# Kernel optimization log

Hardware: AMD Instinct MI355X
Metric: run time of the kernel (lower is better)

The kernel has to match this reference:

```python
import jax, jax.numpy as jnp
import numpy as np

HEADS = 6
PS = 7  # window size
DN = ('NCHW', 'OIHW', 'NCHW')


def _conv1x1(x, w):
    return jax.lax.conv_general_dilated(x, w, (1, 1), 'VALID', dimension_numbers=DN)


def _dwconv3(x, w, groups):
    return jax.lax.conv_general_dilated(x, w, (1, 1), 'SAME', dimension_numbers=DN,
                                        feature_group_count=groups)


def _l2norm(t, eps=1e-12):
    # matches torch F.normalize(dim=-1): x / max(||x||_2, eps)
    n = jnp.sqrt(jnp.sum(t * t, axis=-1, keepdims=True))
    return t / jnp.maximum(n, eps)


def setup_inputs() -> dict:
    key = jax.random.key(0)
    k1, k2, k3, k4 = jax.random.split(key, 4)
    B, C, H, W = 2, 180, 448, 448
    x = jax.random.normal(k1, (B, C, H, W), dtype=jnp.float32)
    temperature = jnp.ones((HEADS, 1, 1), dtype=jnp.float32)
    w_qkv = jax.random.normal(k2, (3 * C, C, 1, 1), dtype=jnp.float32) * 0.05
    w_dw = jax.random.normal(k3, (3 * C, 1, 3, 3), dtype=jnp.float32) * 0.05
    w_proj = jax.random.normal(k4, (C, C, 1, 1), dtype=jnp.float32) * 0.05
    return {'x': x, 'temperature': temperature, 'w_qkv': w_qkv, 'w_dw': w_dw, 'w_proj': w_proj}


def reference(x, temperature, w_qkv, w_dw, w_proj):
    b, c, H, W = x.shape
    d = c // HEADS
    hh, ww = H // PS, W // PS

    qkv = _dwconv3(_conv1x1(x, w_qkv), w_dw, 3 * c)  # [b, 3c, H, W]
    q, k, v = jnp.split(qkv, 3, axis=1)

    def rearr(t):
        # 'b (head d) (h ph) (w pw) -> b (h w) head d (ph pw)'
        t = t.reshape(b, HEADS, d, hh, PS, ww, PS)
        t = t.transpose(0, 3, 5, 1, 2, 4, 6)  # b, hh, ww, head, d, ph, pw
        return t.reshape(b, hh * ww, HEADS, d, PS * PS)

    q, k, v = rearr(q), rearr(k), rearr(v)
    q = _l2norm(q)
    k = _l2norm(k)

    # channel-channel attention per window: [b, n_win, head, d, d]
    attn = jnp.einsum('bnhdp,bnhep->bnhde', q, k) * temperature
    attn = jax.nn.softmax(attn, axis=-1)
    out = jnp.einsum('bnhde,bnhep->bnhdp', attn, v)

    # inverse rearrange: 'b (h w) head d (ph pw) -> b (head d) (h ph) (w pw)'
    out = out.reshape(b, hh, ww, HEADS, d, PS, PS)
    out = out.transpose(0, 3, 4, 1, 5, 2, 6).reshape(b, c, H, W)
    return _conv1x1(out, w_proj)
```

## Files before the change

kernel.cpp:

```cpp
#include <hip/hip_runtime.h>

#define HW 200704
#define WIMG 448
#define VPLANE 229376

typedef __attribute__((ext_vector_type(4))) unsigned int u32x4;
typedef __attribute__((ext_vector_type(4))) float f32x4;
typedef __attribute__((ext_vector_type(8))) short s16x8;

static __device__ __forceinline__ unsigned short f2bf(float f) {
    union { float f; unsigned int u; } v; v.f = f;
    unsigned int u = v.u;
    unsigned int r = u + 0x7FFFu + ((u >> 16) & 1u);
    return (unsigned short)(r >> 16);
}
static __device__ __forceinline__ float bf2f(unsigned short s) {
    union { unsigned int u; float f; } v; v.u = ((unsigned int)s) << 16;
    return v.f;
}

__global__ __launch_bounds__(256) void wconv_kernel(
    const float* __restrict__ wq, unsigned short* __restrict__ wqb)
{
    int idx = blockIdx.x * 256 + threadIdx.x;
    if (idx >= 576 * 24) return;
    int row = idx / 24, ch = idx - row * 24;
    unsigned short u[8];
#pragma unroll
    for (int e = 0; e < 8; ++e) {
        int k = ch * 8 + e;
        u[e] = (row < 540 && k < 180) ? f2bf(wq[row * 180 + k]) : (unsigned short)0;
    }
    *(u32x4*)(wqb + row * 192 + ch * 8) = *(const u32x4*)u;
}

__global__ __launch_bounds__(256) void transpose_cast_kernel(
    const float* __restrict__ x, unsigned short* __restrict__ xT)
{
    const int p0 = blockIdx.x * 64;
    const int tid = threadIdx.x;
    const int pl = tid & 63;

    __shared__ float T[180 * 65];

    for (int ic = tid >> 6; ic < 180; ic += 4)
        T[ic * 65 + pl] = x[(size_t)ic * HW + p0 + pl];
    __syncthreads();

    const int cg = tid >> 6;
    unsigned short* drow = xT + ((size_t)p0 + pl) * 192;
#pragma unroll
    for (int i = 0; i < 6; ++i) {
        int k0 = (cg * 6 + i) * 8;
        unsigned short u[8];
#pragma unroll
        for (int e = 0; e < 8; ++e)
            u[e] = (k0 + e < 180) ? f2bf(T[(k0 + e) * 65 + pl]) : (unsigned short)0;
        *(u32x4*)(drow + k0) = *(const u32x4*)u;
    }
}

__global__ __launch_bounds__(256) void gemm_qkv_kernel(
    const unsigned short* __restrict__ xT, const unsigned short* __restrict__ wqb,
    unsigned short* __restrict__ A)
{
    const int d    = blockIdx.x;
    const int orig = (d & 7) * 882 + (d >> 3);
    const int pt   = orig / 9;
    const int ocb  = (orig - pt * 9) * 64;
    const int pix0 = pt * 256;
    const int tid  = threadIdx.x;
    const int l    = tid & 63;
    const int q    = tid >> 6;
    const int r15  = l & 15;
    const int g4   = l >> 4;

    __shared__ __align__(16) unsigned short xs[2][256 * 64];

    auto stage = [&](int c, int buf) {
#pragma unroll
        for (int i = 0; i < 8; ++i) {
            int slot = i * 256 + tid;
            int px   = slot >> 3;
            int g    = slot & 7;
            const unsigned short* src =
                xT + ((size_t)pix0 + px) * 192 + c * 64 + ((g ^ (px & 7)) << 3);
            __builtin_amdgcn_global_load_lds(
                (const __attribute__((address_space(1))) unsigned int*)(const void*)src,
                (__attribute__((address_space(3))) unsigned int*)(void*)(&xs[buf][slot * 8]),
                16, 0, 0);
        }
    };

    f32x4 acc[4][4];
#pragma unroll
    for (int nt = 0; nt < 4; ++nt)
#pragma unroll
        for (int mi = 0; mi < 4; ++mi) acc[nt][mi] = (f32x4){0.f, 0.f, 0.f, 0.f};

    const unsigned short* wrow = wqb + (size_t)(ocb + r15) * 192;

    stage(0, 0);
    __syncthreads();

    for (int c = 0; c < 3; ++c) {
        if (c < 2) stage(c + 1, (c + 1) & 1);
        const unsigned short* xb = xs[c & 1];
#pragma unroll
        for (int kk = 0; kk < 2; ++kk) {
            s16x8 aX[4], bW[4];
#pragma unroll
            for (int nt = 0; nt < 4; ++nt) {
                int px = q * 64 + nt * 16 + r15;
                aX[nt] = __builtin_bit_cast(s16x8, *(const u32x4*)(
                    xb + px * 64 + (((kk * 4 + g4) ^ (px & 7)) << 3)));
            }
#pragma unroll
            for (int mi = 0; mi < 4; ++mi)
                bW[mi] = __builtin_bit_cast(s16x8, *(const u32x4*)(
                    wrow + mi * 16 * 192 + c * 64 + kk * 32 + g4 * 8));
#pragma unroll
            for (int nt = 0; nt < 4; ++nt)
#pragma unroll
                for (int mi = 0; mi < 4; ++mi)
                    acc[nt][mi] = __builtin_amdgcn_mfma_f32_16x16x32_bf16(
                        aX[nt], bW[mi], acc[nt][mi], 0, 0, 0);
        }
        if (c < 2) __syncthreads();
    }

#pragma unroll
    for (int mi = 0; mi < 4; ++mi) {
        int oc = ocb + mi * 16 + r15;
        if (oc < 540) {
            unsigned short* orow = A + (size_t)oc * HW + pix0 + q * 64 + g4 * 4;
#pragma unroll
            for (int nt = 0; nt < 4; ++nt) {
                uint2 v;
                v.x = (unsigned int)f2bf(acc[nt][mi][0]) |
                      ((unsigned int)f2bf(acc[nt][mi][1]) << 16);
                v.y = (unsigned int)f2bf(acc[nt][mi][2]) |
                      ((unsigned int)f2bf(acc[nt][mi][3]) << 16);
                *(uint2*)(orow + nt * 16) = v;
            }
        }
    }
}

__global__ __launch_bounds__(256) void dw_kernel(
    const unsigned short* __restrict__ A, const float* __restrict__ wdw,
    unsigned short* __restrict__ Bw)
{
    const int wrow = blockIdx.x;
    const int c    = blockIdx.y;
    const int tid  = threadIdx.x;

    const int part = c / 180;
    const int rem  = c - part * 180;
    const int head = rem / 30;
    const int dc   = rem - head * 30;

    __shared__ float Ls[9 * 452];

    float w9[9];
#pragma unroll
    for (int i = 0; i < 9; ++i) w9[i] = wdw[c * 9 + i];

    const int y0 = wrow * 7;
    const unsigned int* Ac32 = (const unsigned int*)(A + (size_t)c * HW);
    for (int idx = tid; idx < 2016; idx += 256) {
        int r  = idx / 224;
        int c2 = idx - r * 224;
        int y  = y0 + r - 1;
        unsigned int v = ((unsigned)y < 448u) ? Ac32[y * 224 + c2] : 0u;
        Ls[r * 452 + 1 + 2 * c2] = bf2f((unsigned short)(v & 0xffffu));
        Ls[r * 452 + 2 + 2 * c2] = bf2f((unsigned short)(v >> 16));
    }
    if (tid < 18) {
        int r = tid >> 1;
        Ls[r * 452 + ((tid & 1) ? 449 : 0)] = 0.f;
    }
    __syncthreads();

    unsigned int* dst = (unsigned int*)(Bw +
        ((size_t)(head * 3 + part) * 30 + dc) * VPLANE + (size_t)wrow * 64 * 56);
#pragma unroll
    for (int k = 0; k < 7; ++k) {
        int o2 = k * 256 + tid;
        int wo = o2 / 28;
        int r2 = o2 - wo * 28;
        unsigned short r2v[2];
#pragma unroll
        for (int e = 0; e < 2; ++e) {
            int rm = r2 * 2 + e;
            float acc = 0.f;
            if (rm < 49) {
                int ph = rm / 7, pw = rm - ph * 7;
                int xb = wo * 7 + pw;
                const float* L = Ls + ph * 452 + xb;
                acc = w9[0]*L[0] + w9[1]*L[1] + w9[2]*L[2];
                L += 452;
                acc += w9[3]*L[0] + w9[4]*L[1] + w9[5]*L[2];
                L += 452;
                acc += w9[6]*L[0] + w9[7]*L[1] + w9[8]*L[2];
            }
            r2v[e] = (rm < 49) ? f2bf(acc) : (unsigned short)0;
        }
        dst[o2] = (unsigned int)r2v[0] | ((unsigned int)r2v[1] << 16);
    }
}

__global__ __launch_bounds__(256) void attn2_kernel(
    const unsigned short* __restrict__ Bw,
    const float* __restrict__ temperature,
    unsigned short* __restrict__ Cwt)
{
    __shared__ __align__(16) unsigned short lds[4][6144];
    __shared__ float invs[4][64];

    const int w    = threadIdx.x >> 6;
    const int l    = threadIdx.x & 63;
    const int wg   = blockIdx.x;
    const int head = blockIdx.y;
    const int win  = wg * 4 + w;
    const float temp = temperature[head];
    unsigned short* U = lds[w];
    float* inv = invs[w];
    const int r15 = l & 15;
    const int g4  = l >> 4;

    {
        const unsigned short* plane0 =
            Bw + (size_t)(head * 3) * 30 * VPLANE + (size_t)win * 56;
#pragma unroll
        for (int i = 0; i < 8; ++i) {
            int part = i >> 2;
            int row  = ((i & 3) << 3) | (l >> 3);
            int c    = l & 7;
            u32x4 v = {0u, 0u, 0u, 0u};
            if (row < 30 && c < 7)
                v = *(const u32x4*)(plane0 + (size_t)(part * 30 + row) * VPLANE + c * 8);
            *(u32x4*)(U + part * 2048 + row * 64 + ((c ^ (row & 7)) << 3)) = v;
        }
    }
    {
        const unsigned short* vplane =
            Bw + (size_t)(head * 3 + 2) * 30 * VPLANE + (size_t)win * 56;
        for (int j = 0; j < 23; ++j) {
            int idx = j * 64 + l;
            if (idx < 1470) {
                int dc = idx / 49;
                int p  = idx - dc * 49;
                unsigned short val = vplane[(size_t)dc * VPLANE + p];
                int col = (((dc >> 3) ^ (p & 3)) << 3) | (dc & 7);
                U[4096 + p * 32 + col] = val;
            }
        }
        int c30 = ((3 ^ (l & 3)) << 3) | 6;
        U[4096 + l * 32 + c30]     = 0;
        U[4096 + l * 32 + c30 + 1] = 0;
    }
    __syncthreads();

    s16x8 aQ[2][2], bK[2][2];
#pragma unroll
    for (int mi = 0; mi < 2; ++mi)
#pragma unroll
        for (int kk = 0; kk < 2; ++kk) {
            int r  = mi * 16 + r15;
            int gk = kk * 4 + g4;
            int so = ((gk ^ (r & 7)) << 3);
            aQ[mi][kk] = __builtin_bit_cast(s16x8, *(const u32x4*)(U + r * 64 + so));
            bK[mi][kk] = __builtin_bit_cast(s16x8, *(const u32x4*)(U + 2048 + r * 64 + so));
        }

    f32x4 s[2][2], dq[2], dk[2];
#pragma unroll
    for (int mi = 0; mi < 2; ++mi) {
        dq[mi] = (f32x4){0.f, 0.f, 0.f, 0.f};
        dk[mi] = (f32x4){0.f, 0.f, 0.f, 0.f};
#pragma unroll
        for (int nj = 0; nj < 2; ++nj) s[mi][nj] = (f32x4){0.f, 0.f, 0.f, 0.f};
    }

#pragma unroll
    for (int kk = 0; kk < 2; ++kk) {
#pragma unroll
        for (int mi = 0; mi < 2; ++mi) {
#pragma unroll
            for (int nj = 0; nj < 2; ++nj)
                s[mi][nj] = __builtin_amdgcn_mfma_f32_16x16x32_bf16(
                    aQ[mi][kk], bK[nj][kk], s[mi][nj], 0, 0, 0);
            dq[mi] = __builtin_amdgcn_mfma_f32_16x16x32_bf16(
                aQ[mi][kk], aQ[mi][kk], dq[mi], 0, 0, 0);
            dk[mi] = __builtin_amdgcn_mfma_f32_16x16x32_bf16(
                bK[mi][kk], bK[mi][kk], dk[mi], 0, 0, 0);
        }
    }

#pragma unroll
    for (int mi = 0; mi < 2; ++mi)
#pragma unroll
        for (int reg = 0; reg < 4; ++reg) {
            int row = g4 * 4 + reg;
            if (row == r15) {
                inv[mi * 16 + row]      = 1.f / fmaxf(sqrtf(dq[mi][reg]), 1e-12f);
                inv[32 + mi * 16 + row] = 1.f / fmaxf(sqrtf(dk[mi][reg]), 1e-12f);
            }
        }
    __syncthreads();

    float pr[2][2][4];
    float cinvk0 = inv[32 + r15];
    float cinvk1 = inv[32 + 16 + r15];
#pragma unroll
    for (int mi = 0; mi < 2; ++mi)
#pragma unroll
        for (int reg = 0; reg < 4; ++reg) {
            float qi = inv[mi * 16 + g4 * 4 + reg];
            float v0 = s[mi][0][reg] * qi * cinvk0 * temp;
            float v1 = s[mi][1][reg] * qi * cinvk1 * temp;
            if (16 + r15 >= 30) v1 = -1e30f;
            float m = fmaxf(v0, v1);
#pragma unroll
            for (int off = 1; off < 16; off <<= 1) m = fmaxf(m, __shfl_xor(m, off));
            float e0 = __expf(v0 - m);
            float e1 = __expf(v1 - m);
            float sum = e0 + e1;
#pragma unroll
            for (int off = 1; off < 16; off <<= 1) sum += __shfl_xor(sum, off);
            float rs = 1.f / sum;
            pr[mi][0][reg] = e0 * rs;
            pr[mi][1][reg] = e1 * rs;
        }

#pragma unroll
    for (int mi = 0; mi < 2; ++mi)
#pragma unroll
        for (int nj = 0; nj < 2; ++nj)
#pragma unroll
            for (int reg = 0; reg < 4; ++reg) {
                int row = mi * 16 + g4 * 4 + reg;
                int col = nj * 16 + r15;
                int scol = (((col >> 3) ^ (row & 3)) << 3) | (col & 7);
                U[row * 32 + scol] = f2bf(pr[mi][nj][reg]);
            }
    __syncthreads();

    s16x8 aP[2], bV[4];
#pragma unroll
    for (int mi = 0; mi < 2; ++mi) {
        int i = mi * 16 + r15;
        aP[mi] = __builtin_bit_cast(s16x8,
                 *(const u32x4*)(U + i * 32 + ((g4 ^ (i & 3)) << 3)));
    }
#pragma unroll
    for (int nt = 0; nt < 4; ++nt) {
        int p = nt * 16 + r15;
        bV[nt] = __builtin_bit_cast(s16x8,
                 *(const u32x4*)(U + 4096 + p * 32 + ((g4 ^ (p & 3)) << 3)));
    }
    f32x4 o[2][4];
#pragma unroll
    for (int mi = 0; mi < 2; ++mi)
#pragma unroll
        for (int nt = 0; nt < 4; ++nt) {
            o[mi][nt] = (f32x4){0.f, 0.f, 0.f, 0.f};
            o[mi][nt] = __builtin_amdgcn_mfma_f32_16x16x32_bf16(
                aP[mi], bV[nt], o[mi][nt], 0, 0, 0);
        }

    unsigned short* dst = Cwt + ((size_t)win * 49) * 192 + head * 30;
#pragma unroll
    for (int mi = 0; mi < 2; ++mi) {
        int ch0 = mi * 16 + g4 * 4;
#pragma unroll
        for (int nt = 0; nt < 4; ++nt) {
            int p = nt * 16 + r15;
            if (p < 49) {
                unsigned int lo = (unsigned int)f2bf(o[mi][nt][0]) |
                                  ((unsigned int)f2bf(o[mi][nt][1]) << 16);
                *(unsigned int*)(dst + (size_t)p * 192 + ch0) = lo;
                if (ch0 + 2 < 30) {
                    unsigned int hi = (unsigned int)f2bf(o[mi][nt][2]) |
                                      ((unsigned int)f2bf(o[mi][nt][3]) << 16);
                    *(unsigned int*)(dst + (size_t)p * 192 + ch0 + 2) = hi;
                }
            }
        }
    }
    if (head == 5 && g4 == 0) {
        unsigned short* zrow = Cwt + ((size_t)win * 49) * 192 + 180;
#pragma unroll
        for (int nt = 0; nt < 4; ++nt) {
            int p = nt * 16 + r15;
            if (p < 49) {
                *(unsigned int*)(zrow + (size_t)p * 192 + 0) = 0u;
                *(unsigned int*)(zrow + (size_t)p * 192 + 2) = 0u;
                *(unsigned int*)(zrow + (size_t)p * 192 + 4) = 0u;
            }
        }
    }
}

__global__ __launch_bounds__(256) void gemm_proj_kernel(
    const unsigned short* __restrict__ Cwt, const float* __restrict__ wp,
    float* __restrict__ out)
{
    const int d    = blockIdx.x;
    const int orig = (d & 7) * 294 + (d >> 3);
    const int pt   = orig / 3;
    const int ocb  = (orig - pt * 3) * 64;
    const int pix0 = pt * 256;
    const int tid  = threadIdx.x;
    const int l    = tid & 63;
    const int w    = tid >> 6;
    const int r15  = l & 15;
    const int g4   = l >> 4;

    __shared__ __align__(16) unsigned short wlds[64 * 200];
    __shared__ __align__(16) unsigned short xs[256 * 40];

    for (int idx = tid; idx < 64 * 24; idx += 256) {
        int row = idx / 24, ch = idx - (idx / 24) * 24;
        int oc = ocb + row;
        unsigned short u[8];
#pragma unroll
        for (int e = 0; e < 8; ++e) {
            int k = ch * 8 + e;
            u[e] = (oc < 180 && k < 180) ? f2bf(wp[oc * 180 + k]) : (unsigned short)0;
        }
        *(u32x4*)(wlds + row * 200 + ch * 8) = *(const u32x4*)u;
    }

    const unsigned short* srow[4];
#pragma unroll
    for (int i = 0; i < 4; ++i) {
        int P = pix0 + i * 64 + (tid >> 2);
        int win = P / 49, p = P - win * 49;
        srow[i] = Cwt + ((size_t)win * 49 + p) * 192 + (tid & 3) * 8;
    }
    const int sdst = (tid >> 2) * 40 + (tid & 3) * 8;

    f32x4 acc[4][4];
#pragma unroll
    for (int mi = 0; mi < 4; ++mi)
#pragma unroll
        for (int nt = 0; nt < 4; ++nt) acc[mi][nt] = (f32x4){0.f, 0.f, 0.f, 0.f};

    for (int ks = 0; ks < 6; ++ks) {
        __syncthreads();
#pragma unroll
        for (int i = 0; i < 4; ++i)
            *(u32x4*)(xs + sdst + i * 64 * 40) = *(const u32x4*)(srow[i] + ks * 32);
        __syncthreads();

        s16x8 aW[4], bX[4];
#pragma unroll
        for (int mi = 0; mi < 4; ++mi)
            aW[mi] = __builtin_bit_cast(s16x8,
                     *(const u32x4*)(wlds + (mi * 16 + r15) * 200 + ks * 32 + g4 * 8));
#pragma unroll
        for (int nt = 0; nt < 4; ++nt)
            bX[nt] = __builtin_bit_cast(s16x8,
                     *(const u32x4*)(xs + (w * 64 + nt * 16 + r15) * 40 + g4 * 8));
#pragma unroll
        for (int mi = 0; mi < 4; ++mi)
#pragma unroll
            for (int nt = 0; nt < 4; ++nt)
                acc[mi][nt] = __builtin_amdgcn_mfma_f32_16x16x32_bf16(
                    aW[mi], bX[nt], acc[mi][nt], 0, 0, 0);
    }

    int poff[4];
#pragma unroll
    for (int nt = 0; nt < 4; ++nt) {
        int P = pix0 + w * 64 + nt * 16 + r15;
        int win = P / 49, p = P - win * 49;
        int ph = p / 7, pw2 = p - ph * 7;
        poff[nt] = ((win >> 6) * 7 + ph) * WIMG + (win & 63) * 7 + pw2;
    }
#pragma unroll
    for (int mi = 0; mi < 4; ++mi) {
#pragma unroll
        for (int reg = 0; reg < 4; ++reg) {
            int oc = ocb + mi * 16 + g4 * 4 + reg;
            if (oc < 180) {
#pragma unroll
                for (int nt = 0; nt < 4; ++nt)
                    out[(size_t)oc * HW + poff[nt]] = acc[mi][nt][reg];
            }
        }
    }
}

extern "C" void kernel_launch(void* const* d_in, const int* in_sizes, int n_in,
                              void* d_out, int out_size, void* d_ws, size_t ws_size,
                              hipStream_t stream) {
    const float* x           = (const float*)d_in[0];
    const float* temperature = (const float*)d_in[1];
    const float* w_qkv       = (const float*)d_in[2];
    const float* w_dw        = (const float*)d_in[3];
    const float* w_proj      = (const float*)d_in[4];
    float* out = (float*)d_out;

    if (ws_size < 618848256ull) return;
    unsigned short* xT  = (unsigned short*)d_ws;
    unsigned short* A   = (unsigned short*)((char*)d_ws + 77070336ull);
    unsigned short* Bw  = (unsigned short*)((char*)d_ws + 293830656ull);
    unsigned short* Cwt = (unsigned short*)((char*)d_ws + 541556736ull);
    unsigned short* wqb = (unsigned short*)((char*)d_ws + 618627072ull);

    wconv_kernel<<<dim3(54), 256, 0, stream>>>(w_qkv, wqb);

    for (int b = 0; b < 2; ++b) {
        const float* xb = x + (size_t)b * 180 * HW;
        float* ob = out + (size_t)b * 180 * HW;
        transpose_cast_kernel<<<dim3(HW / 64), 256, 0, stream>>>(xb, xT);
        gemm_qkv_kernel<<<dim3(7056), 256, 0, stream>>>(xT, wqb, A);
        dw_kernel<<<dim3(64, 540), 256, 0, stream>>>(A, w_dw, Bw);
        attn2_kernel<<<dim3(1024, 6), 256, 0, stream>>>(Bw, temperature, Cwt);
        gemm_proj_kernel<<<dim3(2352), 256, 0, stream>>>(Cwt, w_proj, ob);
    }
}
```

Before: 1.316 ms.

## Double-buffer proj GEMM with async LDS loads and precast weights

The projection GEMM now reads a weight matrix that is cast to bf16 once up front and loads A fragments straight from global memory, so each block no longer converts weights or stages them in LDS. Activation tiles are staged with global_load_lds into a double-buffered, XOR-swizzled LDS layout in 64-wide K chunks, so the next chunk loads while the current one feeds the MFMAs. This cuts the number of barriers and avoids bank conflicts. The cost is more LDS per block, which may lower occupancy, and weight fragments now come from global or cache memory.

```diff
diff --git a/kernel.cpp b/kernel.cpp
--- a/kernel.cpp
+++ b/kernel.cpp
@@ -20,18 +20,19 @@
 }
 
 __global__ __launch_bounds__(256) void wconv_kernel(
-    const float* __restrict__ wq, unsigned short* __restrict__ wqb)
+    const float* __restrict__ src, unsigned short* __restrict__ dst,
+    int ocu, int octot)
 {
     int idx = blockIdx.x * 256 + threadIdx.x;
-    if (idx >= 576 * 24) return;
+    if (idx >= octot * 24) return;
     int row = idx / 24, ch = idx - row * 24;
     unsigned short u[8];
 #pragma unroll
     for (int e = 0; e < 8; ++e) {
         int k = ch * 8 + e;
-        u[e] = (row < 540 && k < 180) ? f2bf(wq[row * 180 + k]) : (unsigned short)0;
-    }
-    *(u32x4*)(wqb + row * 192 + ch * 8) = *(const u32x4*)u;
+        u[e] = (row < ocu && k < 180) ? f2bf(src[row * 180 + k]) : (unsigned short)0;
+    }
+    *(u32x4*)(dst + row * 192 + ch * 8) = *(const u32x4*)u;
 }
 
 __global__ __launch_bounds__(256) void transpose_cast_kernel(
@@ -404,7 +405,7 @@
 }
 
 __global__ __launch_bounds__(256) void gemm_proj_kernel(
-    const unsigned short* __restrict__ Cwt, const float* __restrict__ wp,
+    const unsigned short* __restrict__ Cwt, const unsigned short* __restrict__ wpb,
     float* __restrict__ out)
 {
     const int d    = blockIdx.x;
@@ -414,33 +415,26 @@
     const int pix0 = pt * 256;
     const int tid  = threadIdx.x;
     const int l    = tid & 63;
-    const int w    = tid >> 6;
+    const int q    = tid >> 6;
     const int r15  = l & 15;
     const int g4   = l >> 4;
 
-    __shared__ __align__(16) unsigned short wlds[64 * 200];
-    __shared__ __align__(16) unsigned short xs[256 * 40];
-
-    for (int idx = tid; idx < 64 * 24; idx += 256) {
-        int row = idx / 24, ch = idx - (idx / 24) * 24;
-        int oc = ocb + row;
-        unsigned short u[8];
-#pragma unroll
-        for (int e = 0; e < 8; ++e) {
-            int k = ch * 8 + e;
-            u[e] = (oc < 180 && k < 180) ? f2bf(wp[oc * 180 + k]) : (unsigned short)0;
-        }
-        *(u32x4*)(wlds + row * 200 + ch * 8) = *(const u32x4*)u;
-    }
-
-    const unsigned short* srow[4];
-#pragma unroll
-    for (int i = 0; i < 4; ++i) {
-        int P = pix0 + i * 64 + (tid >> 2);
-        int win = P / 49, p = P - win * 49;
-        srow[i] = Cwt + ((size_t)win * 49 + p) * 192 + (tid & 3) * 8;
-    }
-    const int sdst = (tid >> 2) * 40 + (tid & 3) * 8;
+    __shared__ __align__(16) unsigned short xs[2][256 * 64];
+
+    auto stage = [&](int c, int buf) {
+#pragma unroll
+        for (int i = 0; i < 8; ++i) {
+            int slot = i * 256 + tid;
+            int px   = slot >> 3;
+            int g    = slot & 7;
+            const unsigned short* src =
+                Cwt + ((size_t)pix0 + px) * 192 + c * 64 + ((g ^ (px & 7)) << 3);
+            __builtin_amdgcn_global_load_lds(
+                (const __attribute__((address_space(1))) unsigned int*)(const void*)src,
+                (__attribute__((address_space(3))) unsigned int*)(void*)(&xs[buf][slot * 8]),
+                16, 0, 0);
+        }
+    };
 
     f32x4 acc[4][4];
 #pragma unroll
@@ -448,34 +442,41 @@
 #pragma unroll
         for (int nt = 0; nt < 4; ++nt) acc[mi][nt] = (f32x4){0.f, 0.f, 0.f, 0.f};
 
-    for (int ks = 0; ks < 6; ++ks) {
-        __syncthreads();
-#pragma unroll
-        for (int i = 0; i < 4; ++i)
-            *(u32x4*)(xs + sdst + i * 64 * 40) = *(const u32x4*)(srow[i] + ks * 32);
-        __syncthreads();
-
-        s16x8 aW[4], bX[4];
-#pragma unroll
-        for (int mi = 0; mi < 4; ++mi)
-            aW[mi] = __builtin_bit_cast(s16x8,
-                     *(const u32x4*)(wlds + (mi * 16 + r15) * 200 + ks * 32 + g4 * 8));
-#pragma unroll
-        for (int nt = 0; nt < 4; ++nt)
-            bX[nt] = __builtin_bit_cast(s16x8,
-                     *(const u32x4*)(xs + (w * 64 + nt * 16 + r15) * 40 + g4 * 8));
-#pragma unroll
-        for (int mi = 0; mi < 4; ++mi)
-#pragma unroll
-            for (int nt = 0; nt < 4; ++nt)
-                acc[mi][nt] = __builtin_amdgcn_mfma_f32_16x16x32_bf16(
-                    aW[mi], bX[nt], acc[mi][nt], 0, 0, 0);
+    const unsigned short* wrow = wpb + (size_t)(ocb + r15) * 192;
+
+    stage(0, 0);
+    __syncthreads();
+
+    for (int c = 0; c < 3; ++c) {
+        if (c < 2) stage(c + 1, (c + 1) & 1);
+        const unsigned short* xb = xs[c & 1];
+#pragma unroll
+        for (int kk = 0; kk < 2; ++kk) {
+            s16x8 aW[4], bX[4];
+#pragma unroll
+            for (int mi = 0; mi < 4; ++mi)
+                aW[mi] = __builtin_bit_cast(s16x8, *(const u32x4*)(
+                    wrow + mi * 16 * 192 + c * 64 + kk * 32 + g4 * 8));
+#pragma unroll
+            for (int nt = 0; nt < 4; ++nt) {
+                int px = q * 64 + nt * 16 + r15;
+                bX[nt] = __builtin_bit_cast(s16x8, *(const u32x4*)(
+                    xb + px * 64 + (((kk * 4 + g4) ^ (px & 7)) << 3)));
+            }
+#pragma unroll
+            for (int mi = 0; mi < 4; ++mi)
+#pragma unroll
+                for (int nt = 0; nt < 4; ++nt)
+                    acc[mi][nt] = __builtin_amdgcn_mfma_f32_16x16x32_bf16(
+                        aW[mi], bX[nt], acc[mi][nt], 0, 0, 0);
+        }
+        if (c < 2) __syncthreads();
     }
 
     int poff[4];
 #pragma unroll
     for (int nt = 0; nt < 4; ++nt) {
-        int P = pix0 + w * 64 + nt * 16 + r15;
+        int P = pix0 + q * 64 + nt * 16 + r15;
         int win = P / 49, p = P - win * 49;
         int ph = p / 7, pw2 = p - ph * 7;
         poff[nt] = ((win >> 6) * 7 + ph) * WIMG + (win & 63) * 7 + pw2;
@@ -504,14 +505,16 @@
     const float* w_proj      = (const float*)d_in[4];
     float* out = (float*)d_out;
 
-    if (ws_size < 618848256ull) return;
+    if (ws_size < 618921984ull) return;
     unsigned short* xT  = (unsigned short*)d_ws;
     unsigned short* A   = (unsigned short*)((char*)d_ws + 77070336ull);
     unsigned short* Bw  = (unsigned short*)((char*)d_ws + 293830656ull);
     unsigned short* Cwt = (unsigned short*)((char*)d_ws + 541556736ull);
     unsigned short* wqb = (unsigned short*)((char*)d_ws + 618627072ull);
-
-    wconv_kernel<<<dim3(54), 256, 0, stream>>>(w_qkv, wqb);
+    unsigned short* wpb = (unsigned short*)((char*)d_ws + 618848256ull);
+
+    wconv_kernel<<<dim3(54), 256, 0, stream>>>(w_qkv, wqb, 540, 576);
+    wconv_kernel<<<dim3(18), 256, 0, stream>>>(w_proj, wpb, 180, 192);
 
     for (int b = 0; b < 2; ++b) {
         const float* xb = x + (size_t)b * 180 * HW;
@@ -520,6 +523,6 @@
         gemm_qkv_kernel<<<dim3(7056), 256, 0, stream>>>(xT, wqb, A);
         dw_kernel<<<dim3(64, 540), 256, 0, stream>>>(A, w_dw, Bw);
         attn2_kernel<<<dim3(1024, 6), 256, 0, stream>>>(Bw, temperature, Cwt);
-        gemm_proj_kernel<<<dim3(2352), 256, 0, stream>>>(Cwt, w_proj, ob);
-    }
-}
+        gemm_proj_kernel<<<dim3(2352), 256, 0, stream>>>(Cwt, wpb, ob);
+    }
+}
```

Result: faster. 1.283 ms (-2.5%).
